# Kernel optimization log

Measured on AMD Instinct MI355X. Metric: run time of the kernel, lower is better.

Reference implementation:

```python
import jax, jax.numpy as jnp
import numpy as np

V = 50000      # vocab size
FEAT = 300     # glove dim
HID = 512      # num_hidden
C = 20         # class_num (GAT feature width)
L = 2          # num_layers
NH = 4         # num_heads
K = 3          # diffusion hops
ALPHA = 0.1    # teleport prob
N = 76800      # total nodes in batched graph
E = 1250000    # total edges
B = 512        # number of graphs (docs)
SLOPE = 0.2    # leaky relu slope (DGL GAT default)


def setup_inputs() -> dict:
    key = jax.random.key(0)
    ks = jax.random.split(key, 12)
    node_ids = jax.random.randint(ks[0], (N,), 0, V)
    edge_src = jax.random.randint(ks[1], (E,), 0, N)
    edge_dst = jax.random.randint(ks[2], (E,), 0, N)
    graph_ids = jnp.sort(jax.random.randint(ks[3], (N,), 0, B))
    emb = jax.random.uniform(ks[4], (V, FEAT), minval=-0.1, maxval=0.1, dtype=jnp.float32)
    W1 = jax.random.normal(ks[5], (FEAT, HID), dtype=jnp.float32) / np.sqrt(FEAT)
    b1 = jnp.zeros((HID,), jnp.float32)
    W2 = jax.random.normal(ks[6], (HID, C), dtype=jnp.float32) / np.sqrt(HID)
    b2 = jnp.zeros((C,), jnp.float32)
    gat_W = jax.random.normal(ks[7], (L, NH, C, C), dtype=jnp.float32) / np.sqrt(C)
    gat_asrc = jax.random.normal(ks[8], (L, NH, C), dtype=jnp.float32) * 0.1
    gat_adst = jax.random.normal(ks[9], (L, NH, C), dtype=jnp.float32) * 0.1
    ws_W = jax.random.normal(ks[10], (C, 1), dtype=jnp.float32) / np.sqrt(C)
    ws_b = jnp.zeros((1,), jnp.float32)
    return {"node_ids": node_ids, "edge_src": edge_src, "edge_dst": edge_dst,
            "graph_ids": graph_ids, "emb": emb, "W1": W1, "b1": b1, "W2": W2,
            "b2": b2, "gat_W": gat_W, "gat_asrc": gat_asrc, "gat_adst": gat_adst,
            "ws_W": ws_W, "ws_b": ws_b}


def _segment_softmax(e, dst, n):
    # e: [NH, E] edge scores; softmax over edges sharing the same destination node
    seg_max = jax.vmap(lambda v: jax.ops.segment_max(v, dst, num_segments=n))(e)
    seg_max = jnp.where(jnp.isfinite(seg_max), seg_max, 0.0)
    ex = jnp.exp(e - seg_max[:, dst])
    denom = jax.vmap(lambda v: jax.ops.segment_sum(v, dst, num_segments=n))(ex)
    return ex / (denom[:, dst] + 1e-9)


def _forward(node_ids, edge_src, edge_dst, graph_ids, emb, W1, b1, W2, b2,
             gat_W, gat_asrc, gat_adst, ws_W, ws_b):
    x = jnp.take(emb, node_ids, axis=0)              # [N, FEAT] embedding lookup
    x = jax.nn.relu(x @ W1 + b1)                     # [N, HID]
    h = x @ W2 + b2                                  # [N, C]
    for l in range(L):
        z = jnp.einsum('nc,hcd->hnd', h, gat_W[l])   # [NH, N, C]
        es = jnp.einsum('hnd,hd->hn', z, gat_asrc[l])
        ed = jnp.einsum('hnd,hd->hn', z, gat_adst[l])
        e = jax.nn.leaky_relu(es[:, edge_src] + ed[:, edge_dst], SLOPE)  # [NH, E]
        att = _segment_softmax(e, edge_dst, N)       # [NH, E]
        # attention diffusion: H <- (1-alpha) * A_att @ H + alpha * H0
        H0 = z
        Hc = z
        for _ in range(K):
            msg = att[:, :, None] * Hc[:, edge_src, :]                     # [NH, E, C]
            agg = jax.vmap(lambda m: jax.ops.segment_sum(m, edge_dst, num_segments=N))(msg)
            Hc = (1.0 - ALPHA) * agg + ALPHA * H0
        h = Hc.mean(axis=0)                          # merge='mean' over heads
        if l < L - 1:
            h = jax.nn.elu(h)
    gate = jax.nn.sigmoid(h @ ws_W + ws_b)           # [N, 1] WeightAndSum gate
    return jax.ops.segment_sum(h * gate, graph_ids, num_segments=B)  # [B, C]


def reference(node_ids, edge_src, edge_dst, graph_ids, emb, W1, b1, W2, b2,
              gat_W, gat_asrc, gat_adst, ws_W, ws_b):
    return _forward(node_ids, edge_src, edge_dst, graph_ids, emb, W1, b1, W2, b2,
                    gat_W, gat_asrc, gat_adst, ws_W, ws_b)
```

## Files before the change

### kernel.cpp

```cpp
#include <hip/hip_runtime.h>
#include <hip/hip_bf16.h>
#include <hip/hip_fp16.h>
#include <math.h>

#define VOCAB 50000
#define FEAT 300
#define KPAD 320
#define HID 512
#define C 20
#define NL 2
#define NH 4
#define KHOP 3
#define ALPHA 0.1f
#define NNODE 76800
#define NEDGE 1250000
#define NB 512
#define SLOPE 0.2f

#define NBKT 300
#define BKTCAP 5120
#define NSLOT (NBKT * BKTCAP)
#define EPB 5120
#define NEBLK ((NEDGE + EPB - 1) / EPB)

#define BM 32
#define VPAD 50048
#define SX_STRIDE 520

typedef float f32x4 __attribute__((ext_vector_type(4)));
typedef short bf16x8 __attribute__((ext_vector_type(8)));

__device__ inline unsigned short f2b(float x) {
  __hip_bfloat16 h = __float2bfloat16(x);
  return *reinterpret_cast<unsigned short*>(&h);
}

union R20 {
  struct { uint4 a, b; uint2 c; } v;
  __half2 h[10];
};
__device__ inline R20 ldrow20(const __half* p) {
  R20 r;
  r.v.a = *(const uint4*)p;
  r.v.b = *(const uint4*)(p + 8);
  r.v.c = *(const uint2*)(p + 16);
  return r;
}
__device__ inline void strow20(__half* p, const R20& r) {
  *(uint4*)p = r.v.a;
  *(uint4*)(p + 8) = r.v.b;
  *(uint2*)(p + 16) = r.v.c;
}

#define H2SWZ(v, pat) ({ union { __half2 h; int i; } _u; _u.h = (v);          \
                         _u.i = __builtin_amdgcn_ds_swizzle(_u.i, (pat));     \
                         _u.h; })
#define FSWZ(x, pat) __int_as_float(                                          \
    __builtin_amdgcn_ds_swizzle(__float_as_int(x), (pat)))
#define SLOTRED_H2(v) do {                                                    \
    v = __hadd2(v, H2SWZ(v, 0x101F));                                         \
    v = __hadd2(v, H2SWZ(v, 0x201F));                                         \
    v = __hadd2(v, H2SWZ(v, 0x401F)); } while (0)

__global__ void k_cvt_w1(const float* __restrict__ W1, ushort* __restrict__ W1t)
{
  int idx = blockIdx.x * 256 + threadIdx.x;
  int kc = idx >> 12;
  int rem = idx & 4095;
  int col = rem >> 3;
  int j = rem & 7;
  int k = kc * 8 + j;
  W1t[idx] = (k < FEAT) ? f2b(W1[(size_t)k * HID + col]) : (ushort)0;
}

__global__ void k_prep_coef(const float* __restrict__ gatW0,
                            const float* __restrict__ as0,
                            const float* __restrict__ ad0,
                            const float* __restrict__ b2,
                            float* __restrict__ coef, float* __restrict__ bb)
{
  int col = threadIdx.x;
  if (col >= 96) return;
  float cf[C];
  if (col < 80) {
    int hd = col / C, d = col - hd * C;
#pragma unroll
    for (int j = 0; j < C; j++) cf[j] = gatW0[(hd * C + j) * C + d];
  } else if (col < 88) {
    int hd = col - 80;
#pragma unroll
    for (int j = 0; j < C; j++) {
      float s = 0.f;
#pragma unroll
      for (int d = 0; d < C; d++) s += gatW0[(hd * C + j) * C + d] * as0[hd * C + d];
      cf[j] = s;
    }
  } else {
    int hd = col - 88;
#pragma unroll
    for (int j = 0; j < C; j++) {
      float s = 0.f;
#pragma unroll
      for (int d = 0; d < C; d++) s += gatW0[(hd * C + j) * C + d] * ad0[hd * C + d];
      cf[j] = s;
    }
  }
  float bbv = 0.f;
#pragma unroll
  for (int j = 0; j < C; j++) { coef[col * C + j] = cf[j]; bbv += b2[j] * cf[j]; }
  bb[col] = bbv;
}

__global__ void k_prep_wcp(const float* __restrict__ W2,
                           const float* __restrict__ coef,
                           ushort* __restrict__ Wcpt)
{
  int idx = blockIdx.x * 256 + threadIdx.x;
  int kc = idx / 768;
  int rem = idx - kc * 768;
  int col = rem >> 3;
  int j = rem & 7;
  int k = kc * 8 + j;
  float s = 0.f;
#pragma unroll
  for (int jj = 0; jj < C; jj++) s += W2[(size_t)k * C + jj] * coef[col * C + jj];
  Wcpt[idx] = f2b(s);
}

__global__ __launch_bounds__(512, 6) void k_mlp_mfma(
    const float* __restrict__ emb, const ushort* __restrict__ W1t,
    const float* __restrict__ b1, const ushort* __restrict__ Wcpt,
    const float* __restrict__ bb, __half* __restrict__ zfull,
    float* __restrict__ esf, float* __restrict__ edf)
{
  __shared__ ushort smem[16640];
  ushort* sA = smem;
  ushort* sX = smem;

  const int t = threadIdx.x;
  const int lane = t & 63;
  const int w = t >> 6;
  const int v0 = blockIdx.x * BM;
  const int l15 = lane & 15;
  const int l4 = lane >> 4;
  const int cb = w * 64;

#pragma unroll
  for (int j = 0; j < 3; j++) {
    int chunk = j * 512 + t;
    if (chunk < 1280) {
      int row = chunk & 31;
      int kc = chunk >> 5;
      int vr = v0 + row;
      if (vr >= VOCAB) vr = VOCAB - 1;
      int k0 = kc * 8;
      const float* p = emb + (size_t)vr * FEAT + k0;
      ushort u[8];
      if (k0 + 8 <= FEAT) {
        float4 x = *(const float4*)p;
        float4 y = *(const float4*)(p + 4);
        u[0] = f2b(x.x); u[1] = f2b(x.y); u[2] = f2b(x.z); u[3] = f2b(x.w);
        u[4] = f2b(y.x); u[5] = f2b(y.y); u[6] = f2b(y.z); u[7] = f2b(y.w);
      } else {
#pragma unroll
        for (int q = 0; q < 8; q++)
          u[q] = (k0 + q < FEAT) ? f2b(p[q]) : (ushort)0;
      }
      *(uint4*)(sA + (size_t)chunk * 8) = *(const uint4*)u;
    }
  }
  __syncthreads();

  f32x4 acc[2][4];
#pragma unroll
  for (int rt = 0; rt < 2; rt++)
#pragma unroll
    for (int ct = 0; ct < 4; ct++) acc[rt][ct] = (f32x4)0.f;

  for (int ks = 0; ks < 10; ks++) {
    const int kcb = ks * 4 + l4;
    bf16x8 a0 = *(const bf16x8*)(sA + ((size_t)kcb * 32 + l15) * 8);
    bf16x8 a1 = *(const bf16x8*)(sA + ((size_t)kcb * 32 + 16 + l15) * 8);
    const ushort* wb = W1t + ((size_t)kcb * 512 + cb + l15) * 8;
    bf16x8 bf[4];
#pragma unroll
    for (int ct = 0; ct < 4; ct++) bf[ct] = *(const bf16x8*)(wb + ct * 128);
#pragma unroll
    for (int ct = 0; ct < 4; ct++) {
      acc[0][ct] = __builtin_amdgcn_mfma_f32_16x16x32_bf16(a0, bf[ct], acc[0][ct], 0, 0, 0);
      acc[1][ct] = __builtin_amdgcn_mfma_f32_16x16x32_bf16(a1, bf[ct], acc[1][ct], 0, 0, 0);
    }
  }
  __syncthreads();

#pragma unroll
  for (int rt = 0; rt < 2; rt++)
#pragma unroll
    for (int ct = 0; ct < 4; ct++) {
      int col = cb + ct * 16 + l15;
      float bias = b1[col];
#pragma unroll
      for (int r4 = 0; r4 < 4; r4++) {
        int row = rt * 16 + l4 * 4 + r4;
        float x = fmaxf(acc[rt][ct][r4] + bias, 0.f);
        sX[(size_t)row * SX_STRIDE + col] = f2b(x);
      }
    }
  __syncthreads();

  const int ntile = (w < 4) ? 2 : 1;
  for (int i = 0; i < ntile; i++) {
    const int tt = (i == 0) ? w : 8 + w;
    const int rt = tt & 1, ct = tt >> 1;
    const ushort* xb = sX + (size_t)(rt * 16 + l15) * SX_STRIDE + l4 * 8;
    const ushort* wbp = Wcpt + ((size_t)l4 * 96 + ct * 16 + l15) * 8;
    bf16x8 bv[16];
#pragma unroll
    for (int ks = 0; ks < 16; ks++)
      bv[ks] = *(const bf16x8*)(wbp + (size_t)ks * 3072);
    f32x4 a2 = (f32x4)0.f;
#pragma unroll
    for (int ks = 0; ks < 16; ks++) {
      bf16x8 av = *(const bf16x8*)(xb + ks * 32);
      a2 = __builtin_amdgcn_mfma_f32_16x16x32_bf16(av, bv[ks], a2, 0, 0, 0);
    }
    const int col = ct * 16 + l15;
    const float bias = bb[col];
#pragma unroll
    for (int r = 0; r < 4; r++) {
      const int vrow = v0 + rt * 16 + l4 * 4 + r;
      if (vrow >= VOCAB) continue;
      float val = a2[r] + bias;
      if (col < 80) {
        int hd = col / C, c = col - hd * C;
        zfull[((size_t)vrow * NH + hd) * 20 + c] = __float2half_rn(val);
      } else if (col < 88) {
        esf[(size_t)vrow * NH + (col - 80)] = val;
      } else {
        edf[(size_t)vrow * NH + (col - 88)] = val;
      }
    }
  }
}

__global__ __launch_bounds__(256) void k_bkt_scatter(
    const int* __restrict__ src, const int* __restrict__ dst,
    int* __restrict__ gcur, int* __restrict__ gbuf)
{
  __shared__ int hist[NBKT];
  __shared__ int lcur[NBKT];
  const int t = threadIdx.x;
  for (int i = t; i < NBKT; i += 256) hist[i] = 0;
  __syncthreads();
  const int base = blockIdx.x * EPB;
#pragma unroll
  for (int j = 0; j < 20; j++) {
    int e = base + j * 256 + t;
    if (e < NEDGE) atomicAdd(&hist[dst[e] >> 8], 1);
  }
  __syncthreads();
  for (int i = t; i < NBKT; i += 256) {
    int v = hist[i];
    lcur[i] = v ? atomicAdd(&gcur[i], v) : 0;
  }
  __syncthreads();
#pragma unroll
  for (int j = 0; j < 20; j++) {
    int e = base + j * 256 + t;
    if (e < NEDGE) {
      int d = dst[e];
      int b = d >> 8;
      int idx = atomicAdd(&lcur[b], 1);
      if (idx < BKTCAP)
        gbuf[(size_t)b * BKTCAP + idx] = (src[e] << 8) | (d & 255);
    }
  }
}

__global__ __launch_bounds__(256) void k_csr_build(
    const int* __restrict__ gcur, const int* __restrict__ gbuf,
    const int* __restrict__ node_ids, int* __restrict__ offs,
    int* __restrict__ deg, int* __restrict__ srcc, int* __restrict__ srcv)
{
  __shared__ int shist[256];
  __shared__ int lcur[256];
  __shared__ int wsum[4];
  const int b = blockIdx.x;
  const int t = threadIdx.x;
  const int base = b * BKTCAP;
  int nb = gcur[b];
  if (nb > BKTCAP) nb = BKTCAP;
  shist[t] = 0;
  __syncthreads();
  for (int i = t; i < nb; i += 256)
    atomicAdd(&shist[gbuf[base + i] & 255], 1);
  __syncthreads();
  int v = shist[t];
  int x = v;
#pragma unroll
  for (int off = 1; off < 64; off <<= 1) {
    int y = __shfl_up(x, off, 64);
    if ((t & 63) >= off) x += y;
  }
  if ((t & 63) == 63) wsum[t >> 6] = x;
  __syncthreads();
  int waveoff = 0;
#pragma unroll
  for (int w = 0; w < 4; w++) waveoff += (w < (t >> 6)) ? wsum[w] : 0;
  int pre = base + waveoff + x - v;
  offs[b * 256 + t] = pre;
  deg[b * 256 + t] = v;
  lcur[t] = pre;
  __syncthreads();
  for (int i = t; i < nb; i += 256) {
    int p = gbuf[base + i];
    int slot = atomicAdd(&lcur[p & 255], 1);
    int s = p >> 8;
    srcc[slot] = s;
    srcv[slot] = node_ids[s];
  }
}

__global__ __launch_bounds__(256) void k_hop_first(
    const int* __restrict__ offs, const int* __restrict__ deg,
    const int* __restrict__ sidx,
    const float* __restrict__ esT, const float* __restrict__ edT,
    const int* __restrict__ ids, const __half* __restrict__ Zt,
    __half* __restrict__ att, float* __restrict__ invden,
    __half* __restrict__ Hout)
{
  const int t = threadIdx.x;
  const int head = t & 3;
  const int eslot = (t >> 2) & 7;
  const int n = blockIdx.x * 8 + (t >> 5);
  const int g = n * NH + head;
  const int idn = ids ? ids[n] : n;
  const int beg = offs[n], end = beg + deg[n];
  const float edv = edT[(size_t)idn * NH + head];
  __half2 agg[10];
#pragma unroll
  for (int q = 0; q < 10; q++) agg[q] = __floats2half2_rn(0.f, 0.f);
  float den = 0.f;
  int p = beg + eslot;
  while (p + 8 < end) {
    int sv0 = sidx[p];
    int sv1 = sidx[p + 8];
    float es0 = esT[(size_t)sv0 * NH + head];
    float es1 = esT[(size_t)sv1 * NH + head];
    R20 r0 = ldrow20(Zt + ((size_t)sv0 * NH + head) * 20);
    R20 r1 = ldrow20(Zt + ((size_t)sv1 * NH + head) * 20);
    float e0 = es0 + edv; e0 = e0 > 0.f ? e0 : SLOPE * e0;
    float e1 = es1 + edv; e1 = e1 > 0.f ? e1 : SLOPE * e1;
    float ex0 = __expf(e0), ex1 = __expf(e1);
    att[(size_t)p * NH + head] = __float2half_rn(ex0);
    att[(size_t)(p + 8) * NH + head] = __float2half_rn(ex1);
    den += ex0 + ex1;
    __half2 a0 = __float2half2_rn(ex0);
    __half2 a1 = __float2half2_rn(ex1);
#pragma unroll
    for (int q = 0; q < 10; q++) {
      agg[q] = __hfma2(a0, r0.h[q], agg[q]);
      agg[q] = __hfma2(a1, r1.h[q], agg[q]);
    }
    p += 16;
  }
  if (p < end) {
    int sv0 = sidx[p];
    float es0 = esT[(size_t)sv0 * NH + head];
    R20 r0 = ldrow20(Zt + ((size_t)sv0 * NH + head) * 20);
    float e0 = es0 + edv; e0 = e0 > 0.f ? e0 : SLOPE * e0;
    float ex0 = __expf(e0);
    att[(size_t)p * NH + head] = __float2half_rn(ex0);
    den += ex0;
    __half2 a0 = __float2half2_rn(ex0);
#pragma unroll
    for (int q = 0; q < 10; q++) agg[q] = __hfma2(a0, r0.h[q], agg[q]);
  }
#pragma unroll
  for (int q = 0; q < 10; q++) SLOTRED_H2(agg[q]);
  den += FSWZ(den, 0x101F);
  den += FSWZ(den, 0x201F);
  den += FSWZ(den, 0x401F);
  if (eslot == 0) {
    float inv = 1.f / (den + 1e-9f);
    invden[g] = inv;
    R20 h0 = ldrow20(Zt + ((size_t)idn * NH + head) * 20);
    __half2 s2 = __float2half2_rn(inv * (1.0f - ALPHA));
    __half2 al = __float2half2_rn(ALPHA);
    R20 o;
#pragma unroll
    for (int q = 0; q < 10; q++)
      o.h[q] = __hfma2(s2, agg[q], __hmul2(al, h0.h[q]));
    strow20(Hout + (size_t)g * 20, o);
  }
}

__global__ __launch_bounds__(256) void k_hop_mid(
    const int* __restrict__ offs, const int* __restrict__ deg,
    const int* __restrict__ srcc,
    const __half* __restrict__ att, const float* __restrict__ invden,
    const __half* __restrict__ Hin, const __half* __restrict__ Zt,
    const int* __restrict__ ids, __half* __restrict__ Hout)
{
  const int t = threadIdx.x;
  const int head = t & 3;
  const int eslot = (t >> 2) & 7;
  const int n = blockIdx.x * 8 + (t >> 5);
  const int g = n * NH + head;
  const int idn = ids ? ids[n] : n;
  const int beg = offs[n], end = beg + deg[n];
  __half2 agg[10];
#pragma unroll
  for (int q = 0; q < 10; q++) agg[q] = __floats2half2_rn(0.f, 0.f);
  int p = beg + eslot;
  while (p + 8 < end) {
    __half a0h = att[(size_t)p * NH + head];
    __half a1h = att[(size_t)(p + 8) * NH + head];
    int sn0 = srcc[p];
    int sn1 = srcc[p + 8];
    R20 r0 = ldrow20(Hin + ((size_t)sn0 * NH + head) * 20);
    R20 r1 = ldrow20(Hin + ((size_t)sn1 * NH + head) * 20);
    __half2 a0 = __half2half2(a0h);
    __half2 a1 = __half2half2(a1h);
#pragma unroll
    for (int q = 0; q < 10; q++) {
      agg[q] = __hfma2(a0, r0.h[q], agg[q]);
      agg[q] = __hfma2(a1, r1.h[q], agg[q]);
    }
    p += 16;
  }
  if (p < end) {
    __half a0h = att[(size_t)p * NH + head];
    int sn0 = srcc[p];
    R20 r0 = ldrow20(Hin + ((size_t)sn0 * NH + head) * 20);
    __half2 a0 = __half2half2(a0h);
#pragma unroll
    for (int q = 0; q < 10; q++) agg[q] = __hfma2(a0, r0.h[q], agg[q]);
  }
#pragma unroll
  for (int q = 0; q < 10; q++) SLOTRED_H2(agg[q]);
  if (eslot == 0) {
    R20 h0 = ldrow20(Zt + ((size_t)idn * NH + head) * 20);
    __half2 s2 = __float2half2_rn(invden[g] * (1.0f - ALPHA));
    __half2 al = __float2half2_rn(ALPHA);
    R20 o;
#pragma unroll
    for (int q = 0; q < 10; q++)
      o.h[q] = __hfma2(s2, agg[q], __hmul2(al, h0.h[q]));
    strow20(Hout + (size_t)g * 20, o);
  }
}

__global__ __launch_bounds__(256) void k_hop_last_proj(
    const int* __restrict__ offs, const int* __restrict__ deg,
    const int* __restrict__ srcc,
    const __half* __restrict__ att, const float* __restrict__ invden,
    const __half* __restrict__ Hin, const __half* __restrict__ Zt,
    const int* __restrict__ ids,
    const float* __restrict__ gatW1, const float* __restrict__ as1,
    const float* __restrict__ ad1,
    __half* __restrict__ zb, float* __restrict__ es, float* __restrict__ ed)
{
  __shared__ float sW[NH * C * C];
  __shared__ float sa[NH * C], sd[NH * C];
  const int t = threadIdx.x;
  for (int i = t; i < NH * C * C; i += 256) sW[i] = gatW1[i];
  if (t < NH * C) { sa[t] = as1[t]; sd[t] = ad1[t]; }
  __syncthreads();

  const int head = t & 3;
  const int eslot = (t >> 2) & 7;
  const int n = blockIdx.x * 8 + (t >> 5);
  const int g = n * NH + head;
  const int idn = ids ? ids[n] : n;
  const int beg = offs[n], end = beg + deg[n];
  __half2 agg[10];
#pragma unroll
  for (int q = 0; q < 10; q++) agg[q] = __floats2half2_rn(0.f, 0.f);
  int p = beg + eslot;
  while (p + 8 < end) {
    __half a0h = att[(size_t)p * NH + head];
    __half a1h = att[(size_t)(p + 8) * NH + head];
    int sn0 = srcc[p];
    int sn1 = srcc[p + 8];
    R20 r0 = ldrow20(Hin + ((size_t)sn0 * NH + head) * 20);
    R20 r1 = ldrow20(Hin + ((size_t)sn1 * NH + head) * 20);
    __half2 a0 = __half2half2(a0h);
    __half2 a1 = __half2half2(a1h);
#pragma unroll
    for (int q = 0; q < 10; q++) {
      agg[q] = __hfma2(a0, r0.h[q], agg[q]);
      agg[q] = __hfma2(a1, r1.h[q], agg[q]);
    }
    p += 16;
  }
  if (p < end) {
    __half a0h = att[(size_t)p * NH + head];
    int sn0 = srcc[p];
    R20 r0 = ldrow20(Hin + ((size_t)sn0 * NH + head) * 20);
    __half2 a0 = __half2half2(a0h);
#pragma unroll
    for (int q = 0; q < 10; q++) agg[q] = __hfma2(a0, r0.h[q], agg[q]);
  }
#pragma unroll
  for (int q = 0; q < 10; q++) SLOTRED_H2(agg[q]);

  R20 h0 = ldrow20(Zt + ((size_t)idn * NH + head) * 20);
  __half2 s2 = __float2half2_rn(invden[g] * (1.0f - ALPHA));
  __half2 al = __float2half2_rn(ALPHA);
  float o[C];
#pragma unroll
  for (int q = 0; q < 10; q++) {
    __half2 m = __hfma2(s2, agg[q], __hmul2(al, h0.h[q]));
    m = __hadd2(m, H2SWZ(m, 0x041F));
    m = __hadd2(m, H2SWZ(m, 0x081F));
    float2 f = __half22float2(m);
    float v0 = f.x * 0.25f, v1 = f.y * 0.25f;
    o[2 * q]     = v0 > 0.f ? v0 : __expf(v0) - 1.f;
    o[2 * q + 1] = v1 > 0.f ? v1 : __expf(v1) - 1.f;
  }

  const float* Wh = &sW[head * C * C];
  float esp = 0.f, edp = 0.f;
#pragma unroll
  for (int j = 0; j < 3; j++) {
    int d = eslot + j * 8;
    if (d < C) {
      float zv = 0.f;
#pragma unroll
      for (int c = 0; c < C; c++) zv += o[c] * Wh[c * C + d];
      esp += zv * sa[head * C + d];
      edp += zv * sd[head * C + d];
      zb[((size_t)n * NH + head) * 20 + d] = __float2half_rn(zv);
    }
  }
  esp += FSWZ(esp, 0x101F);
  esp += FSWZ(esp, 0x201F);
  esp += FSWZ(esp, 0x401F);
  edp += FSWZ(edp, 0x101F);
  edp += FSWZ(edp, 0x201F);
  edp += FSWZ(edp, 0x401F);
  if (eslot == 0) {
    es[g] = esp;
    ed[g] = edp;
  }
}

#define RSPAN 16
__global__ __launch_bounds__(256) void k_hop_last_final(
    const int* __restrict__ offs, const int* __restrict__ deg,
    const int* __restrict__ srcc,
    const __half* __restrict__ att, const float* __restrict__ invden,
    const __half* __restrict__ Hin, const __half* __restrict__ Zt,
    const int* __restrict__ gids, const float* __restrict__ wsW,
    const float* __restrict__ wsb, float* __restrict__ out)
{
  __shared__ float sacc[RSPAN * C];
  __shared__ int sgmin;
  const int t = threadIdx.x;
  const int head = t & 3;
  const int eslot = (t >> 2) & 7;
  const int n = blockIdx.x * 8 + (t >> 5);
  const int g = n * NH + head;
  const int beg = offs[n], end = beg + deg[n];
  for (int i = t; i < RSPAN * C; i += 256) sacc[i] = 0.f;
  if (t == 0) sgmin = gids[blockIdx.x * 8];
  __syncthreads();
  __half2 agg[10];
#pragma unroll
  for (int q = 0; q < 10; q++) agg[q] = __floats2half2_rn(0.f, 0.f);
  int p = beg + eslot;
  while (p + 8 < end) {
    __half a0h = att[(size_t)p * NH + head];
    __half a1h = att[(size_t)(p + 8) * NH + head];
    int sn0 = srcc[p];
    int sn1 = srcc[p + 8];
    R20 r0 = ldrow20(Hin + ((size_t)sn0 * NH + head) * 20);
    R20 r1 = ldrow20(Hin + ((size_t)sn1 * NH + head) * 20);
    __half2 a0 = __half2half2(a0h);
    __half2 a1 = __half2half2(a1h);
#pragma unroll
    for (int q = 0; q < 10; q++) {
      agg[q] = __hfma2(a0, r0.h[q], agg[q]);
      agg[q] = __hfma2(a1, r1.h[q], agg[q]);
    }
    p += 16;
  }
  if (p < end) {
    __half a0h = att[(size_t)p * NH + head];
    int sn0 = srcc[p];
    R20 r0 = ldrow20(Hin + ((size_t)sn0 * NH + head) * 20);
    __half2 a0 = __half2half2(a0h);
#pragma unroll
    for (int q = 0; q < 10; q++) agg[q] = __hfma2(a0, r0.h[q], agg[q]);
  }
#pragma unroll
  for (int q = 0; q < 10; q++) SLOTRED_H2(agg[q]);
  if (eslot == 0) {
    R20 h0 = ldrow20(Zt + ((size_t)n * NH + head) * 20);
    __half2 s2 = __float2half2_rn(invden[g] * (1.0f - ALPHA));
    __half2 al = __float2half2_rn(ALPHA);
    float o[C];
#pragma unroll
    for (int q = 0; q < 10; q++) {
      __half2 m = __hfma2(s2, agg[q], __hmul2(al, h0.h[q]));
      m = __hadd2(m, H2SWZ(m, 0x041F));
      m = __hadd2(m, H2SWZ(m, 0x081F));
      float2 f = __half22float2(m);
      o[2 * q]     = f.x * 0.25f;
      o[2 * q + 1] = f.y * 0.25f;
    }
    float dotp = 0.f;
#pragma unroll
    for (int j = 0; j < 5; j++) {
      int c = head * 5 + j;
      dotp += o[c] * wsW[c];
    }
    dotp += FSWZ(dotp, 0x041F);
    dotp += FSWZ(dotp, 0x081F);
    const float gate = 1.f / (1.f + __expf(-(dotp + wsb[0])));
    const int b = gids[n];
    const int lb = b - sgmin;
    if (lb < RSPAN) {
#pragma unroll
      for (int j = 0; j < 5; j++) {
        int c = head * 5 + j;
        atomicAdd(&sacc[lb * C + c], o[c] * gate);
      }
    } else {
#pragma unroll
      for (int j = 0; j < 5; j++) {
        int c = head * 5 + j;
        atomicAdd(&out[(size_t)b * C + c], o[c] * gate);
      }
    }
  }
  __syncthreads();
  for (int i = t; i < RSPAN * C; i += 256) {
    float v = sacc[i];
    if (v != 0.f) atomicAdd(&out[(size_t)(sgmin + i / C) * C + (i - (i / C) * C)], v);
  }
}

extern "C" void kernel_launch(void* const* d_in, const int* in_sizes, int n_in,
                              void* d_out, int out_size, void* d_ws, size_t ws_size,
                              hipStream_t stream)
{
  const int*   node_ids = (const int*)  d_in[0];
  const int*   edge_src = (const int*)  d_in[1];
  const int*   edge_dst = (const int*)  d_in[2];
  const int*   graph_ids= (const int*)  d_in[3];
  const float* emb      = (const float*)d_in[4];
  const float* W1       = (const float*)d_in[5];
  const float* b1       = (const float*)d_in[6];
  const float* W2       = (const float*)d_in[7];
  const float* b2       = (const float*)d_in[8];
  const float* gat_W    = (const float*)d_in[9];
  const float* gat_asrc = (const float*)d_in[10];
  const float* gat_adst = (const float*)d_in[11];
  const float* ws_W     = (const float*)d_in[12];
  const float* ws_b     = (const float*)d_in[13];
  float* out = (float*)d_out;

  float* esf    = (float*)d_ws;
  float* edf    = esf   + (size_t)VPAD * NH;
  float* es     = edf   + (size_t)VPAD * NH;
  float* ed     = es    + (size_t)NNODE * NH;
  float* invden = ed    + (size_t)NNODE * NH;
  float* bb     = invden+ (size_t)NNODE * NH;
  float* coef   = bb + 96;
  int*   offs   = (int*)(coef + 96 * C);
  int*   deg    = offs + NNODE;
  int*   gcur   = deg + NNODE;
  int*   srcc   = gcur + NBKT;
  int*   srcv   = srcc + NSLOT;
  uintptr_t a16 = ((uintptr_t)(srcv + NSLOT) + 15) & ~(uintptr_t)15;
  __half* zfull = (__half*)a16;
  __half* zb    = zfull + (size_t)VPAD * NH * 20;
  __half* bufA  = zb    + (size_t)NNODE * NH * 20;
  __half* bufB  = bufA  + (size_t)NNODE * NH * 20;
  ushort* W1t   = (ushort*)(bufB + (size_t)NNODE * NH * 20);
  ushort* Wcpt  = W1t + (size_t)40 * 512 * 8;
  uintptr_t x16 = ((uintptr_t)(Wcpt + 64 * 96 * 8) + 15) & ~(uintptr_t)15;
  int*    gbuf  = (int*)x16;
  __half* att   = (__half*)x16;

  hipMemsetAsync(out, 0, (size_t)NB * C * sizeof(float), stream);
  hipMemsetAsync(gcur, 0, NBKT * sizeof(int), stream);

  k_cvt_w1<<<(40 * 512 * 8) / 256, 256, 0, stream>>>(W1, W1t);
  k_prep_coef<<<1, 128, 0, stream>>>(gat_W, gat_asrc, gat_adst, b2, coef, bb);
  k_prep_wcp<<<(64 * 96 * 8) / 256, 256, 0, stream>>>(W2, coef, Wcpt);

  k_bkt_scatter<<<NEBLK, 256, 0, stream>>>(edge_src, edge_dst, gcur, gbuf);
  k_csr_build<<<NBKT, 256, 0, stream>>>(gcur, gbuf, node_ids,
                                        offs, deg, srcc, srcv);

  k_mlp_mfma<<<VPAD / BM, 512, 0, stream>>>(emb, W1t, b1, Wcpt, bb,
                                            zfull, esf, edf);

  const int HB = NNODE / 8;
  k_hop_first<<<HB, 256, 0, stream>>>(offs, deg, srcv, esf, edf, node_ids,
                                      zfull, att, invden, bufA);
  k_hop_mid<<<HB, 256, 0, stream>>>(offs, deg, srcc, att, invden, bufA, zfull,
                                    node_ids, bufB);
  k_hop_last_proj<<<HB, 256, 0, stream>>>(offs, deg, srcc, att, invden, bufB,
                                          zfull, node_ids,
                                          gat_W + (size_t)NH * C * C,
                                          gat_asrc + NH * C, gat_adst + NH * C,
                                          zb, es, ed);
  k_hop_first<<<HB, 256, 0, stream>>>(offs, deg, srcc, es, ed,
                                      (const int*)nullptr, zb, att, invden,
                                      bufA);
  k_hop_mid<<<HB, 256, 0, stream>>>(offs, deg, srcc, att, invden, bufA, zb,
                                    (const int*)nullptr, bufB);
  k_hop_last_final<<<HB, 256, 0, stream>>>(offs, deg, srcc, att, invden, bufB,
                                           zb, graph_ids, ws_W, ws_b, out);
}
```

Measured before the change: 402.7 us.

## Switch hop kernels to head-major layout and split head merge into separate kernels

After: 501.7 us. +24.6%, slower.

```diff
diff --git a/kernel.cpp b/kernel.cpp
--- a/kernel.cpp
+++ b/kernel.cpp
@@ -26,6 +26,7 @@
 #define BM 32
 #define VPAD 50048
 #define SX_STRIDE 520
+#define NBH (NNODE / 32)
 
 typedef float f32x4 __attribute__((ext_vector_type(4)));
 typedef short bf16x8 __attribute__((ext_vector_type(8)));
@@ -58,9 +59,9 @@
 #define FSWZ(x, pat) __int_as_float(                                          \
     __builtin_amdgcn_ds_swizzle(__float_as_int(x), (pat)))
 #define SLOTRED_H2(v) do {                                                    \
-    v = __hadd2(v, H2SWZ(v, 0x101F));                                         \
-    v = __hadd2(v, H2SWZ(v, 0x201F));                                         \
-    v = __hadd2(v, H2SWZ(v, 0x401F)); } while (0)
+    v = __hadd2(v, H2SWZ(v, 0x041F));                                         \
+    v = __hadd2(v, H2SWZ(v, 0x081F));                                         \
+    v = __hadd2(v, H2SWZ(v, 0x101F)); } while (0)
 
 __global__ void k_cvt_w1(const float* __restrict__ W1, ushort* __restrict__ W1t)
 {
@@ -233,11 +234,11 @@
       float val = a2[r] + bias;
       if (col < 80) {
         int hd = col / C, c = col - hd * C;
-        zfull[((size_t)vrow * NH + hd) * 20 + c] = __float2half_rn(val);
+        zfull[((size_t)hd * VPAD + vrow) * 20 + c] = __float2half_rn(val);
       } else if (col < 88) {
-        esf[(size_t)vrow * NH + (col - 80)] = val;
+        esf[(size_t)(col - 80) * VPAD + vrow] = val;
       } else {
-        edf[(size_t)vrow * NH + (col - 88)] = val;
+        edf[(size_t)(col - 88) * VPAD + vrow] = val;
       }
     }
   }
@@ -327,33 +328,35 @@
     const float* __restrict__ esT, const float* __restrict__ edT,
     const int* __restrict__ ids, const __half* __restrict__ Zt,
     __half* __restrict__ att, float* __restrict__ invden,
-    __half* __restrict__ Hout)
+    __half* __restrict__ Hout, int tstride)
 {
   const int t = threadIdx.x;
-  const int head = t & 3;
-  const int eslot = (t >> 2) & 7;
-  const int n = blockIdx.x * 8 + (t >> 5);
-  const int g = n * NH + head;
+  const int slot = t & 7;
+  const int head = blockIdx.x / NBH;
+  const int n = (blockIdx.x - head * NBH) * 32 + (t >> 3);
   const int idn = ids ? ids[n] : n;
   const int beg = offs[n], end = beg + deg[n];
-  const float edv = edT[(size_t)idn * NH + head];
+  const float* esH = esT + (size_t)head * tstride;
+  const __half* ZH = Zt + (size_t)head * tstride * 20;
+  __half* attH = att + (size_t)head * NSLOT;
+  const float edv = edT[(size_t)head * tstride + idn];
   __half2 agg[10];
 #pragma unroll
   for (int q = 0; q < 10; q++) agg[q] = __floats2half2_rn(0.f, 0.f);
   float den = 0.f;
-  int p = beg + eslot;
+  int p = beg + slot;
   while (p + 8 < end) {
     int sv0 = sidx[p];
     int sv1 = sidx[p + 8];
-    float es0 = esT[(size_t)sv0 * NH + head];
-    float es1 = esT[(size_t)sv1 * NH + head];
-    R20 r0 = ldrow20(Zt + ((size_t)sv0 * NH + head) * 20);
-    R20 r1 = ldrow20(Zt + ((size_t)sv1 * NH + head) * 20);
+    float es0 = esH[sv0];
+    float es1 = esH[sv1];
+    R20 r0 = ldrow20(ZH + (size_t)sv0 * 20);
+    R20 r1 = ldrow20(ZH + (size_t)sv1 * 20);
     float e0 = es0 + edv; e0 = e0 > 0.f ? e0 : SLOPE * e0;
     float e1 = es1 + edv; e1 = e1 > 0.f ? e1 : SLOPE * e1;
     float ex0 = __expf(e0), ex1 = __expf(e1);
-    att[(size_t)p * NH + head] = __float2half_rn(ex0);
-    att[(size_t)(p + 8) * NH + head] = __float2half_rn(ex1);
+    attH[p] = __float2half_rn(ex0);
+    attH[p + 8] = __float2half_rn(ex1);
     den += ex0 + ex1;
     __half2 a0 = __float2half2_rn(ex0);
     __half2 a1 = __float2half2_rn(ex1);
@@ -366,11 +369,11 @@
   }
   if (p < end) {
     int sv0 = sidx[p];
-    float es0 = esT[(size_t)sv0 * NH + head];
-    R20 r0 = ldrow20(Zt + ((size_t)sv0 * NH + head) * 20);
+    float es0 = esH[sv0];
+    R20 r0 = ldrow20(ZH + (size_t)sv0 * 20);
     float e0 = es0 + edv; e0 = e0 > 0.f ? e0 : SLOPE * e0;
     float ex0 = __expf(e0);
-    att[(size_t)p * NH + head] = __float2half_rn(ex0);
+    attH[p] = __float2half_rn(ex0);
     den += ex0;
     __half2 a0 = __float2half2_rn(ex0);
 #pragma unroll
@@ -378,20 +381,20 @@
   }
 #pragma unroll
   for (int q = 0; q < 10; q++) SLOTRED_H2(agg[q]);
+  den += FSWZ(den, 0x041F);
+  den += FSWZ(den, 0x081F);
   den += FSWZ(den, 0x101F);
-  den += FSWZ(den, 0x201F);
-  den += FSWZ(den, 0x401F);
-  if (eslot == 0) {
+  if (slot == 0) {
     float inv = 1.f / (den + 1e-9f);
-    invden[g] = inv;
-    R20 h0 = ldrow20(Zt + ((size_t)idn * NH + head) * 20);
+    invden[(size_t)head * NNODE + n] = inv;
+    R20 h0 = ldrow20(ZH + (size_t)idn * 20);
     __half2 s2 = __float2half2_rn(inv * (1.0f - ALPHA));
     __half2 al = __float2half2_rn(ALPHA);
     R20 o;
 #pragma unroll
     for (int q = 0; q < 10; q++)
       o.h[q] = __hfma2(s2, agg[q], __hmul2(al, h0.h[q]));
-    strow20(Hout + (size_t)g * 20, o);
+    strow20(Hout + ((size_t)head * NNODE + n) * 20, o);
   }
 }
 
@@ -400,26 +403,27 @@
     const int* __restrict__ srcc,
     const __half* __restrict__ att, const float* __restrict__ invden,
     const __half* __restrict__ Hin, const __half* __restrict__ Zt,
-    const int* __restrict__ ids, __half* __restrict__ Hout)
+    const int* __restrict__ ids, __half* __restrict__ Hout, int tstride)
 {
   const int t = threadIdx.x;
-  const int head = t & 3;
-  const int eslot = (t >> 2) & 7;
-  const int n = blockIdx.x * 8 + (t >> 5);
-  const int g = n * NH + head;
+  const int slot = t & 7;
+  const int head = blockIdx.x / NBH;
+  const int n = (blockIdx.x - head * NBH) * 32 + (t >> 3);
   const int idn = ids ? ids[n] : n;
   const int beg = offs[n], end = beg + deg[n];
+  const __half* HH = Hin + (size_t)head * NNODE * 20;
+  const __half* attH = att + (size_t)head * NSLOT;
   __half2 agg[10];
 #pragma unroll
   for (int q = 0; q < 10; q++) agg[q] = __floats2half2_rn(0.f, 0.f);
-  int p = beg + eslot;
+  int p = beg + slot;
   while (p + 8 < end) {
-    __half a0h = att[(size_t)p * NH + head];
-    __half a1h = att[(size_t)(p + 8) * NH + head];
+    __half a0h = attH[p];
+    __half a1h = attH[p + 8];
     int sn0 = srcc[p];
     int sn1 = srcc[p + 8];
-    R20 r0 = ldrow20(Hin + ((size_t)sn0 * NH + head) * 20);
-    R20 r1 = ldrow20(Hin + ((size_t)sn1 * NH + head) * 20);
+    R20 r0 = ldrow20(HH + (size_t)sn0 * 20);
+    R20 r1 = ldrow20(HH + (size_t)sn1 * 20);
     __half2 a0 = __half2half2(a0h);
     __half2 a1 = __half2half2(a1h);
 #pragma unroll
@@ -430,35 +434,30 @@
     p += 16;
   }
   if (p < end) {
-    __half a0h = att[(size_t)p * NH + head];
+    __half a0h = attH[p];
     int sn0 = srcc[p];
-    R20 r0 = ldrow20(Hin + ((size_t)sn0 * NH + head) * 20);
+    R20 r0 = ldrow20(HH + (size_t)sn0 * 20);
     __half2 a0 = __half2half2(a0h);
 #pragma unroll
     for (int q = 0; q < 10; q++) agg[q] = __hfma2(a0, r0.h[q], agg[q]);
   }
 #pragma unroll
   for (int q = 0; q < 10; q++) SLOTRED_H2(agg[q]);
-  if (eslot == 0) {
-    R20 h0 = ldrow20(Zt + ((size_t)idn * NH + head) * 20);
-    __half2 s2 = __float2half2_rn(invden[g] * (1.0f - ALPHA));
+  if (slot == 0) {
+    R20 h0 = ldrow20(Zt + ((size_t)head * tstride + idn) * 20);
+    __half2 s2 = __float2half2_rn(invden[(size_t)head * NNODE + n] * (1.0f - ALPHA));
     __half2 al = __float2half2_rn(ALPHA);
     R20 o;
 #pragma unroll
     for (int q = 0; q < 10; q++)
       o.h[q] = __hfma2(s2, agg[q], __hmul2(al, h0.h[q]));
-    strow20(Hout + (size_t)g * 20, o);
-  }
-}
-
-__global__ __launch_bounds__(256) void k_hop_last_proj(
-    const int* __restrict__ offs, const int* __restrict__ deg,
-    const int* __restrict__ srcc,
-    const __half* __restrict__ att, const float* __restrict__ invden,
-    const __half* __restrict__ Hin, const __half* __restrict__ Zt,
-    const int* __restrict__ ids,
-    const float* __restrict__ gatW1, const float* __restrict__ as1,
-    const float* __restrict__ ad1,
+    strow20(Hout + ((size_t)head * NNODE + n) * 20, o);
+  }
+}
+
+__global__ __launch_bounds__(256) void k_merge_proj(
+    const __half* __restrict__ HL, const float* __restrict__ gatW1,
+    const float* __restrict__ as1, const float* __restrict__ ad1,
     __half* __restrict__ zb, float* __restrict__ es, float* __restrict__ ed)
 {
   __shared__ float sW[NH * C * C];
@@ -467,173 +466,90 @@
   for (int i = t; i < NH * C * C; i += 256) sW[i] = gatW1[i];
   if (t < NH * C) { sa[t] = as1[t]; sd[t] = ad1[t]; }
   __syncthreads();
-
-  const int head = t & 3;
-  const int eslot = (t >> 2) & 7;
-  const int n = blockIdx.x * 8 + (t >> 5);
-  const int g = n * NH + head;
-  const int idn = ids ? ids[n] : n;
-  const int beg = offs[n], end = beg + deg[n];
-  __half2 agg[10];
-#pragma unroll
-  for (int q = 0; q < 10; q++) agg[q] = __floats2half2_rn(0.f, 0.f);
-  int p = beg + eslot;
-  while (p + 8 < end) {
-    __half a0h = att[(size_t)p * NH + head];
-    __half a1h = att[(size_t)(p + 8) * NH + head];
-    int sn0 = srcc[p];
-    int sn1 = srcc[p + 8];
-    R20 r0 = ldrow20(Hin + ((size_t)sn0 * NH + head) * 20);
-    R20 r1 = ldrow20(Hin + ((size_t)sn1 * NH + head) * 20);
-    __half2 a0 = __half2half2(a0h);
-    __half2 a1 = __half2half2(a1h);
+  const int n = blockIdx.x * 256 + t;
+  float o[C];
+  {
+    R20 r0 = ldrow20(HL + ((size_t)0 * NNODE + n) * 20);
+    R20 r1 = ldrow20(HL + ((size_t)1 * NNODE + n) * 20);
+    R20 r2 = ldrow20(HL + ((size_t)2 * NNODE + n) * 20);
+    R20 r3 = ldrow20(HL + ((size_t)3 * NNODE + n) * 20);
 #pragma unroll
     for (int q = 0; q < 10; q++) {
-      agg[q] = __hfma2(a0, r0.h[q], agg[q]);
-      agg[q] = __hfma2(a1, r1.h[q], agg[q]);
-    }
-    p += 16;
-  }
-  if (p < end) {
-    __half a0h = att[(size_t)p * NH + head];
-    int sn0 = srcc[p];
-    R20 r0 = ldrow20(Hin + ((size_t)sn0 * NH + head) * 20);
-    __half2 a0 = __half2half2(a0h);
-#pragma unroll
-    for (int q = 0; q < 10; q++) agg[q] = __hfma2(a0, r0.h[q], agg[q]);
-  }
-#pragma unroll
-  for (int q = 0; q < 10; q++) SLOTRED_H2(agg[q]);
-
-  R20 h0 = ldrow20(Zt + ((size_t)idn * NH + head) * 20);
-  __half2 s2 = __float2half2_rn(invden[g] * (1.0f - ALPHA));
-  __half2 al = __float2half2_rn(ALPHA);
-  float o[C];
-#pragma unroll
-  for (int q = 0; q < 10; q++) {
-    __half2 m = __hfma2(s2, agg[q], __hmul2(al, h0.h[q]));
-    m = __hadd2(m, H2SWZ(m, 0x041F));
-    m = __hadd2(m, H2SWZ(m, 0x081F));
-    float2 f = __half22float2(m);
-    float v0 = f.x * 0.25f, v1 = f.y * 0.25f;
-    o[2 * q]     = v0 > 0.f ? v0 : __expf(v0) - 1.f;
-    o[2 * q + 1] = v1 > 0.f ? v1 : __expf(v1) - 1.f;
-  }
-
-  const float* Wh = &sW[head * C * C];
-  float esp = 0.f, edp = 0.f;
-#pragma unroll
-  for (int j = 0; j < 3; j++) {
-    int d = eslot + j * 8;
-    if (d < C) {
-      float zv = 0.f;
-#pragma unroll
-      for (int c = 0; c < C; c++) zv += o[c] * Wh[c * C + d];
-      esp += zv * sa[head * C + d];
-      edp += zv * sd[head * C + d];
-      zb[((size_t)n * NH + head) * 20 + d] = __float2half_rn(zv);
-    }
-  }
-  esp += FSWZ(esp, 0x101F);
-  esp += FSWZ(esp, 0x201F);
-  esp += FSWZ(esp, 0x401F);
-  edp += FSWZ(edp, 0x101F);
-  edp += FSWZ(edp, 0x201F);
-  edp += FSWZ(edp, 0x401F);
-  if (eslot == 0) {
-    es[g] = esp;
-    ed[g] = edp;
+      float2 f0 = __half22float2(r0.h[q]);
+      float2 f1 = __half22float2(r1.h[q]);
+      float2 f2 = __half22float2(r2.h[q]);
+      float2 f3 = __half22float2(r3.h[q]);
+      float v0 = (f0.x + f1.x + f2.x + f3.x) * 0.25f;
+      float v1 = (f0.y + f1.y + f2.y + f3.y) * 0.25f;
+      o[2 * q]     = v0 > 0.f ? v0 : __expf(v0) - 1.f;
+      o[2 * q + 1] = v1 > 0.f ? v1 : __expf(v1) - 1.f;
+    }
+  }
+#pragma unroll
+  for (int h = 0; h < NH; h++) {
+    const float* Wh = &sW[h * C * C];
+    float esv = 0.f, edv = 0.f;
+    R20 zr;
+#pragma unroll
+    for (int q = 0; q < 10; q++) {
+      float z0 = 0.f, z1 = 0.f;
+      int d0 = 2 * q, d1 = 2 * q + 1;
+#pragma unroll
+      for (int c = 0; c < C; c++) {
+        z0 += o[c] * Wh[c * C + d0];
+        z1 += o[c] * Wh[c * C + d1];
+      }
+      esv += z0 * sa[h * C + d0] + z1 * sa[h * C + d1];
+      edv += z0 * sd[h * C + d0] + z1 * sd[h * C + d1];
+      zr.h[q] = __floats2half2_rn(z0, z1);
+    }
+    strow20(zb + ((size_t)h * NNODE + n) * 20, zr);
+    es[(size_t)h * NNODE + n] = esv;
+    ed[(size_t)h * NNODE + n] = edv;
   }
 }
 
 #define RSPAN 16
-__global__ __launch_bounds__(256) void k_hop_last_final(
-    const int* __restrict__ offs, const int* __restrict__ deg,
-    const int* __restrict__ srcc,
-    const __half* __restrict__ att, const float* __restrict__ invden,
-    const __half* __restrict__ Hin, const __half* __restrict__ Zt,
-    const int* __restrict__ gids, const float* __restrict__ wsW,
-    const float* __restrict__ wsb, float* __restrict__ out)
+__global__ __launch_bounds__(256) void k_merge_readout(
+    const __half* __restrict__ HL, const int* __restrict__ gids,
+    const float* __restrict__ wsW, const float* __restrict__ wsb,
+    float* __restrict__ out)
 {
   __shared__ float sacc[RSPAN * C];
   __shared__ int sgmin;
   const int t = threadIdx.x;
-  const int head = t & 3;
-  const int eslot = (t >> 2) & 7;
-  const int n = blockIdx.x * 8 + (t >> 5);
-  const int g = n * NH + head;
-  const int beg = offs[n], end = beg + deg[n];
+  const int n = blockIdx.x * 256 + t;
   for (int i = t; i < RSPAN * C; i += 256) sacc[i] = 0.f;
-  if (t == 0) sgmin = gids[blockIdx.x * 8];
-  __syncthreads();
-  __half2 agg[10];
-#pragma unroll
-  for (int q = 0; q < 10; q++) agg[q] = __floats2half2_rn(0.f, 0.f);
-  int p = beg + eslot;
-  while (p + 8 < end) {
-    __half a0h = att[(size_t)p * NH + head];
-    __half a1h = att[(size_t)(p + 8) * NH + head];
-    int sn0 = srcc[p];
-    int sn1 = srcc[p + 8];
-    R20 r0 = ldrow20(Hin + ((size_t)sn0 * NH + head) * 20);
-    R20 r1 = ldrow20(Hin + ((size_t)sn1 * NH + head) * 20);
-    __half2 a0 = __half2half2(a0h);
-    __half2 a1 = __half2half2(a1h);
+  if (t == 0) sgmin = gids[blockIdx.x * 256];
+  __syncthreads();
+  float o[C];
+  float dot = wsb[0];
+  {
+    R20 r0 = ldrow20(HL + ((size_t)0 * NNODE + n) * 20);
+    R20 r1 = ldrow20(HL + ((size_t)1 * NNODE + n) * 20);
+    R20 r2 = ldrow20(HL + ((size_t)2 * NNODE + n) * 20);
+    R20 r3 = ldrow20(HL + ((size_t)3 * NNODE + n) * 20);
 #pragma unroll
     for (int q = 0; q < 10; q++) {
-      agg[q] = __hfma2(a0, r0.h[q], agg[q]);
-      agg[q] = __hfma2(a1, r1.h[q], agg[q]);
-    }
-    p += 16;
-  }
-  if (p < end) {
-    __half a0h = att[(size_t)p * NH + head];
-    int sn0 = srcc[p];
-    R20 r0 = ldrow20(Hin + ((size_t)sn0 * NH + head) * 20);
-    __half2 a0 = __half2half2(a0h);
-#pragma unroll
-    for (int q = 0; q < 10; q++) agg[q] = __hfma2(a0, r0.h[q], agg[q]);
-  }
-#pragma unroll
-  for (int q = 0; q < 10; q++) SLOTRED_H2(agg[q]);
-  if (eslot == 0) {
-    R20 h0 = ldrow20(Zt + ((size_t)n * NH + head) * 20);
-    __half2 s2 = __float2half2_rn(invden[g] * (1.0f - ALPHA));
-    __half2 al = __float2half2_rn(ALPHA);
-    float o[C];
-#pragma unroll
-    for (int q = 0; q < 10; q++) {
-      __half2 m = __hfma2(s2, agg[q], __hmul2(al, h0.h[q]));
-      m = __hadd2(m, H2SWZ(m, 0x041F));
-      m = __hadd2(m, H2SWZ(m, 0x081F));
-      float2 f = __half22float2(m);
-      o[2 * q]     = f.x * 0.25f;
-      o[2 * q + 1] = f.y * 0.25f;
-    }
-    float dotp = 0.f;
-#pragma unroll
-    for (int j = 0; j < 5; j++) {
-      int c = head * 5 + j;
-      dotp += o[c] * wsW[c];
-    }
-    dotp += FSWZ(dotp, 0x041F);
-    dotp += FSWZ(dotp, 0x081F);
-    const float gate = 1.f / (1.f + __expf(-(dotp + wsb[0])));
-    const int b = gids[n];
-    const int lb = b - sgmin;
-    if (lb < RSPAN) {
-#pragma unroll
-      for (int j = 0; j < 5; j++) {
-        int c = head * 5 + j;
-        atomicAdd(&sacc[lb * C + c], o[c] * gate);
-      }
-    } else {
-#pragma unroll
-      for (int j = 0; j < 5; j++) {
-        int c = head * 5 + j;
-        atomicAdd(&out[(size_t)b * C + c], o[c] * gate);
-      }
-    }
+      float2 f0 = __half22float2(r0.h[q]);
+      float2 f1 = __half22float2(r1.h[q]);
+      float2 f2 = __half22float2(r2.h[q]);
+      float2 f3 = __half22float2(r3.h[q]);
+      o[2 * q]     = (f0.x + f1.x + f2.x + f3.x) * 0.25f;
+      o[2 * q + 1] = (f0.y + f1.y + f2.y + f3.y) * 0.25f;
+    }
+  }
+#pragma unroll
+  for (int c = 0; c < C; c++) dot += o[c] * wsW[c];
+  const float gate = 1.f / (1.f + __expf(-dot));
+  const int b = gids[n];
+  const int lb = b - sgmin;
+  if (lb < RSPAN) {
+#pragma unroll
+    for (int c = 0; c < C; c++) atomicAdd(&sacc[lb * C + c], o[c] * gate);
+  } else {
+#pragma unroll
+    for (int c = 0; c < C; c++) atomicAdd(&out[(size_t)b * C + c], o[c] * gate);
   }
   __syncthreads();
   for (int i = t; i < RSPAN * C; i += 256) {
@@ -663,11 +579,11 @@
   float* out = (float*)d_out;
 
   float* esf    = (float*)d_ws;
-  float* edf    = esf   + (size_t)VPAD * NH;
-  float* es     = edf   + (size_t)VPAD * NH;
-  float* ed     = es    + (size_t)NNODE * NH;
-  float* invden = ed    + (size_t)NNODE * NH;
-  float* bb     = invden+ (size_t)NNODE * NH;
+  float* edf    = esf   + (size_t)NH * VPAD;
+  float* es     = edf   + (size_t)NH * VPAD;
+  float* ed     = es    + (size_t)NH * NNODE;
+  float* invden = ed    + (size_t)NH * NNODE;
+  float* bb     = invden+ (size_t)NH * NNODE;
   float* coef   = bb + 96;
   int*   offs   = (int*)(coef + 96 * C);
   int*   deg    = offs + NNODE;
@@ -676,10 +592,10 @@
   int*   srcv   = srcc + NSLOT;
   uintptr_t a16 = ((uintptr_t)(srcv + NSLOT) + 15) & ~(uintptr_t)15;
   __half* zfull = (__half*)a16;
-  __half* zb    = zfull + (size_t)VPAD * NH * 20;
-  __half* bufA  = zb    + (size_t)NNODE * NH * 20;
-  __half* bufB  = bufA  + (size_t)NNODE * NH * 20;
-  ushort* W1t   = (ushort*)(bufB + (size_t)NNODE * NH * 20);
+  __half* zb    = zfull + (size_t)NH * VPAD * 20;
+  __half* bufA  = zb    + (size_t)NH * NNODE * 20;
+  __half* bufB  = bufA  + (size_t)NH * NNODE * 20;
+  ushort* W1t   = (ushort*)(bufB + (size_t)NH * NNODE * 20);
   ushort* Wcpt  = W1t + (size_t)40 * 512 * 8;
   uintptr_t x16 = ((uintptr_t)(Wcpt + 64 * 96 * 8) + 15) & ~(uintptr_t)15;
   int*    gbuf  = (int*)x16;
@@ -699,21 +615,25 @@
   k_mlp_mfma<<<VPAD / BM, 512, 0, stream>>>(emb, W1t, b1, Wcpt, bb,
                                             zfull, esf, edf);
 
-  const int HB = NNODE / 8;
+  const int HB = NH * NBH;
   k_hop_first<<<HB, 256, 0, stream>>>(offs, deg, srcv, esf, edf, node_ids,
-                                      zfull, att, invden, bufA);
-  k_hop_mid<<<HB, 256, 0, stream>>>(offs, deg, srcc, att, invden, bufA, zfull,
-                                    node_ids, bufB);
-  k_hop_last_proj<<<HB, 256, 0, stream>>>(offs, deg, srcc, att, invden, bufB,
-                                          zfull, node_ids,
-                                          gat_W + (size_t)NH * C * C,
-                                          gat_asrc + NH * C, gat_adst + NH * C,
-                                          zb, es, ed);
+                                      zfull, att, invden, bufA, VPAD);
+  k_hop_mid<<<HB, 256, 0, stream>>>(offs, deg, srcc, att, invden, bufA,
+                                    zfull, node_ids, bufB, VPAD);
+  k_hop_mid<<<HB, 256, 0, stream>>>(offs, deg, srcc, att, invden, bufB,
+                                    zfull, node_ids, bufA, VPAD);
+  k_merge_proj<<<NNODE / 256, 256, 0, stream>>>(bufA,
+                                                gat_W + (size_t)NH * C * C,
+                                                gat_asrc + NH * C,
+                                                gat_adst + NH * C,
+                                                zb, es, ed);
   k_hop_first<<<HB, 256, 0, stream>>>(offs, deg, srcc, es, ed,
                                       (const int*)nullptr, zb, att, invden,
-                                      bufA);
-  k_hop_mid<<<HB, 256, 0, stream>>>(offs, deg, srcc, att, invden, bufA, zb,
-                                    (const int*)nullptr, bufB);
-  k_hop_last_final<<<HB, 256, 0, stream>>>(offs, deg, srcc, att, invden, bufB,
-                                           zb, graph_ids, ws_W, ws_b, out);
-}
+                                      bufA, NNODE);
+  k_hop_mid<<<HB, 256, 0, stream>>>(offs, deg, srcc, att, invden, bufA,
+                                    zb, (const int*)nullptr, bufB, NNODE);
+  k_hop_mid<<<HB, 256, 0, stream>>>(offs, deg, srcc, att, invden, bufB,
+                                    zb, (const int*)nullptr, bufA, NNODE);
+  k_merge_readout<<<NNODE / 256, 256, 0, stream>>>(bufA, graph_ids,
+                                                   ws_W, ws_b, out);
+}
```
